# Performance work log

Hardware: AMD Instinct MI355X
Metric: run time of the kernel (lower is better)

## Reference

```python
import jax, jax.numpy as jnp
import numpy as np

N, F_IN, H, C, E = 100000, 128, 64, 40, 1600000
NEG_SLOPE = 0.2


def setup_inputs() -> dict:
    key = jax.random.key(0)
    ks = jax.random.split(key, 12)
    s = 0.1
    return {
        "x": jax.random.normal(ks[0], (N, F_IN), jnp.float32),
        "edge_index": jax.random.randint(ks[1], (2, E), 0, N, jnp.int32),
        "W1": jax.random.normal(ks[2], (F_IN, H), jnp.float32) * s,
        "a_src1": jax.random.normal(ks[3], (H,), jnp.float32) * s,
        "a_dst1": jax.random.normal(ks[4], (H,), jnp.float32) * s,
        "b1": jnp.zeros((H,), jnp.float32),
        "W2": jax.random.normal(ks[5], (H, H), jnp.float32) * s,
        "a_src2": jax.random.normal(ks[6], (H,), jnp.float32) * s,
        "a_dst2": jax.random.normal(ks[7], (H,), jnp.float32) * s,
        "b2": jnp.zeros((H,), jnp.float32),
        "Wl": jax.random.normal(ks[8], (H, C), jnp.float32) * s,
        "bl": jnp.zeros((C,), jnp.float32),
    }


def gat_conv(x, src, dst, W, a_src, a_dst, b):
    # PyG GATConv, heads=1, self-loops already appended to (src, dst)
    h = x @ W                                   # [N, H]
    alpha_s = h @ a_src                         # [N]
    alpha_d = h @ a_dst                         # [N]
    e = jax.nn.leaky_relu(alpha_s[src] + alpha_d[dst], NEG_SLOPE)  # [E]
    # segment softmax over incoming edges of each target node
    m = jax.ops.segment_max(e, dst, num_segments=x.shape[0])
    ex = jnp.exp(e - m[dst])
    denom = jax.ops.segment_sum(ex, dst, num_segments=x.shape[0])
    w = ex / (denom[dst] + 1e-16)               # [E]
    out = jax.ops.segment_sum(h[src] * w[:, None], dst, num_segments=x.shape[0])
    return out + b


def reference(x, edge_index, W1, a_src1, a_dst1, b1, W2, a_src2, a_dst2, b2, Wl, bl):
    n = x.shape[0]
    loops = jnp.arange(n, dtype=edge_index.dtype)
    src = jnp.concatenate([edge_index[0], loops])
    dst = jnp.concatenate([edge_index[1], loops])
    h = gat_conv(x, src, dst, W1, a_src1, a_dst1, b1)
    h = jax.nn.relu(h)  # dropout p=0 -> identity
    h = gat_conv(h, src, dst, W2, a_src2, a_dst2, b2)
    logits = h @ Wl + bl
    return jax.nn.log_softmax(logits, axis=-1)
```

## Files before the change

kernel.cpp:

```cpp
#include <hip/hip_runtime.h>
#include <math.h>


#define NEG_SLOPE 0.2f
#define NEG_BIG -3.0e38f

#define BSHIFT 9
#define BSIZE 512
#define BCAP 12288
#define EPB 4096

typedef __bf16 bf16x8 __attribute__((ext_vector_type(8)));
typedef __bf16 bf16x4 __attribute__((ext_vector_type(4)));
typedef float f32x4 __attribute__((ext_vector_type(4)));

__device__ __forceinline__ float lrelu(float x) {
    return x >= 0.f ? x : NEG_SLOPE * x;
}

__device__ __forceinline__ int wave_incl_scan(int v, int lane) {
#pragma unroll
    for (int d = 1; d < 64; d <<= 1) {
        int t = __shfl_up(v, d, 64);
        if (lane >= d) v += t;
    }
    return v;
}


__global__ __launch_bounds__(256) void fused_scatter_gemm(
        const int* __restrict__ src, const int* __restrict__ dst,
        int* __restrict__ bucketCount, unsigned* __restrict__ ebuf, int E, int SB,
        const float* __restrict__ X, const float* __restrict__ W,
        const float* __restrict__ a_src, const float* __restrict__ a_dst,
        __bf16* __restrict__ Hout, float* __restrict__ as_, float* __restrict__ ad_,
        int N, int nTiles) {
    constexpr int K = 128;
    __shared__ __bf16 Whi[64][K + 8];
    __shared__ __bf16 Wlo[64][K + 8];
    __shared__ int hist[256], base[256], cur[256];

    if (blockIdx.x < (unsigned)SB) {
        const int t = threadIdx.x;
        hist[t] = 0;
        __syncthreads();
        const int e0 = blockIdx.x * EPB;
        const int e1 = min(e0 + EPB, E);
        for (int e = e0 + t; e < e1; e += 256)
            atomicAdd(&hist[dst[e] >> BSHIFT], 1);
        __syncthreads();
        if (hist[t] > 0) base[t] = atomicAdd(&bucketCount[t], hist[t]);
        cur[t] = 0;
        __syncthreads();
        for (int e = e0 + t; e < e1; e += 256) {
            int d = dst[e];
            int b = d >> BSHIFT;
            int r = atomicAdd(&cur[b], 1);
            ebuf[(size_t)b * BCAP + base[b] + r] =
                ((unsigned)src[e] << BSHIFT) | (unsigned)(d & (BSIZE - 1));
        }
        return;
    }

    const int gbid = blockIdx.x - SB;
    for (int idx = threadIdx.x; idx < K * 64; idx += 256) {
        int k = idx >> 6, n = idx & 63;
        float w = W[idx];
        __bf16 hi = (__bf16)w;
        Whi[n][k] = hi;
        Wlo[n][k] = (__bf16)(w - (float)hi);
    }
    __syncthreads();

    const int lane  = threadIdx.x & 63;
    const int wave  = threadIdx.x >> 6;
    const int row16 = lane & 15;
    const int quad  = lane >> 4;

    float asv[4], adv[4];
#pragma unroll
    for (int t = 0; t < 4; ++t) {
        asv[t] = a_src[t * 16 + row16];
        adv[t] = a_dst[t * 16 + row16];
    }

    for (int tile = gbid; tile < nTiles; tile += 1024) {
        const int nbase = tile * 64;
        int gn = nbase + wave * 16 + row16;
        if (gn >= N) gn = N - 1;
        const float* __restrict__ xp = X + (size_t)gn * K + quad * 8;

        float4 xv[K / 16];
#pragma unroll
        for (int c = 0; c < K / 32; ++c) {
            xv[2 * c]     = *(const float4*)(xp + c * 32);
            xv[2 * c + 1] = *(const float4*)(xp + c * 32 + 4);
        }

        f32x4 acc[4] = {{0.f, 0.f, 0.f, 0.f}, {0.f, 0.f, 0.f, 0.f},
                        {0.f, 0.f, 0.f, 0.f}, {0.f, 0.f, 0.f, 0.f}};
#pragma unroll
        for (int kc = 0; kc < K; kc += 32) {
            float xs[8];
            *(float4*)&xs[0] = xv[kc / 16];
            *(float4*)&xs[4] = xv[kc / 16 + 1];
            bf16x8 ahi, alo;
#pragma unroll
            for (int j = 0; j < 8; ++j) {
                __bf16 hi = (__bf16)xs[j];
                ahi[j] = hi;
                alo[j] = (__bf16)(xs[j] - (float)hi);
            }
#pragma unroll
            for (int t = 0; t < 4; ++t) {
                bf16x8 bhi = *(const bf16x8*)&Whi[t * 16 + row16][kc + quad * 8];
                bf16x8 blo = *(const bf16x8*)&Wlo[t * 16 + row16][kc + quad * 8];
                acc[t] = __builtin_amdgcn_mfma_f32_16x16x32_bf16(ahi, bhi, acc[t], 0, 0, 0);
                acc[t] = __builtin_amdgcn_mfma_f32_16x16x32_bf16(ahi, blo, acc[t], 0, 0, 0);
                acc[t] = __builtin_amdgcn_mfma_f32_16x16x32_bf16(alo, bhi, acc[t], 0, 0, 0);
            }
        }

        float ps[4] = {0.f, 0.f, 0.f, 0.f};
        float pd[4] = {0.f, 0.f, 0.f, 0.f};
#pragma unroll
        for (int t = 0; t < 4; ++t) {
#pragma unroll
            for (int r = 0; r < 4; ++r) {
                int gm = nbase + wave * 16 + quad * 4 + r;
                if (gm < N) Hout[(size_t)gm * 64 + t * 16 + row16] = (__bf16)acc[t][r];
                ps[r] = fmaf(acc[t][r], asv[t], ps[r]);
                pd[r] = fmaf(acc[t][r], adv[t], pd[r]);
            }
        }
#pragma unroll
        for (int r = 0; r < 4; ++r) {
#pragma unroll
            for (int d = 1; d < 16; d <<= 1) {
                ps[r] += __shfl_xor(ps[r], d, 64);
                pd[r] += __shfl_xor(pd[r], d, 64);
            }
        }
        if (row16 == 0) {
#pragma unroll
            for (int r = 0; r < 4; ++r) {
                int gm = nbase + wave * 16 + quad * 4 + r;
                if (gm < N) { as_[gm] = ps[r]; ad_[gm] = pd[r]; }
            }
        }
    }
}


__global__ __launch_bounds__(512) void bucket_csr(const unsigned* __restrict__ ebuf,
                                                  const int* __restrict__ bucketCount,
                                                  int* __restrict__ offs,
                                                  int* __restrict__ csr, int N, int E) {
    __shared__ int hist[512], cursor[512], wsum[8];
    const int b = blockIdx.x;
    const int t = threadIdx.x;
    const int lane = t & 63;
    const int w = t >> 6;

    int v = (t < 256 && t < b) ? bucketCount[t] : 0;
#pragma unroll
    for (int d = 32; d; d >>= 1) v += __shfl_xor(v, d, 64);
    if (lane == 0) wsum[w] = v;
    hist[t] = 0;
    __syncthreads();
    int gbase = 0;
#pragma unroll
    for (int i = 0; i < 8; ++i) gbase += wsum[i];
    const int cnt = bucketCount[b];
    if (b == 0 && t == 0) offs[N] = E;

    const unsigned* __restrict__ eb = ebuf + (size_t)b * BCAP;
    for (int i = t; i < cnt; i += 512)
        atomicAdd(&hist[eb[i] & (BSIZE - 1)], 1);
    __syncthreads();

    int hv = hist[t];
    int incl = wave_incl_scan(hv, lane);
    if (lane == 63) wsum[w] = incl;
    __syncthreads();
    int prefix = 0;
    for (int i = 0; i < 8; ++i) prefix += (i < w) ? wsum[i] : 0;
    int excl = incl - hv + prefix;
    int n = b * BSIZE + t;
    if (n < N) offs[n] = gbase + excl;
    cursor[t] = excl;
    __syncthreads();

    for (int i = t; i < cnt; i += 512) {
        unsigned rec = eb[i];
        int pos = atomicAdd(&cursor[rec & (BSIZE - 1)], 1);
        csr[gbase + pos] = (int)(rec >> BSHIFT);
    }
}


__global__ __launch_bounds__(256) void gemm_mfma2(const __bf16* __restrict__ X,
                                                  const float* __restrict__ W,
                                                  const float* __restrict__ a_src,
                                                  const float* __restrict__ a_dst,
                                                  __bf16* __restrict__ Hout,
                                                  float* __restrict__ as_,
                                                  float* __restrict__ ad_,
                                                  int N, int nTiles) {
    constexpr int K = 64;
    __shared__ __bf16 Whi[64][K + 8];
    __shared__ __bf16 Wlo[64][K + 8];
    for (int idx = threadIdx.x; idx < K * 64; idx += 256) {
        int k = idx >> 6, n = idx & 63;
        float w = W[idx];
        __bf16 hi = (__bf16)w;
        Whi[n][k] = hi;
        Wlo[n][k] = (__bf16)(w - (float)hi);
    }
    __syncthreads();

    const int lane  = threadIdx.x & 63;
    const int wave  = threadIdx.x >> 6;
    const int row16 = lane & 15;
    const int quad  = lane >> 4;

    float asv[4], adv[4];
#pragma unroll
    for (int t = 0; t < 4; ++t) {
        asv[t] = a_src[t * 16 + row16];
        adv[t] = a_dst[t * 16 + row16];
    }

    for (int tile = blockIdx.x; tile < nTiles; tile += gridDim.x) {
        const int nbase = tile * 64;
        int gn = nbase + wave * 16 + row16;
        if (gn >= N) gn = N - 1;
        const __bf16* __restrict__ xp = X + (size_t)gn * K + quad * 8;
        bf16x8 a0 = *(const bf16x8*)(xp);
        bf16x8 a1 = *(const bf16x8*)(xp + 32);

        f32x4 acc[4] = {{0.f, 0.f, 0.f, 0.f}, {0.f, 0.f, 0.f, 0.f},
                        {0.f, 0.f, 0.f, 0.f}, {0.f, 0.f, 0.f, 0.f}};
#pragma unroll
        for (int kc = 0; kc < K; kc += 32) {
            bf16x8 a = (kc == 0) ? a0 : a1;
#pragma unroll
            for (int t = 0; t < 4; ++t) {
                bf16x8 bhi = *(const bf16x8*)&Whi[t * 16 + row16][kc + quad * 8];
                bf16x8 blo = *(const bf16x8*)&Wlo[t * 16 + row16][kc + quad * 8];
                acc[t] = __builtin_amdgcn_mfma_f32_16x16x32_bf16(a, bhi, acc[t], 0, 0, 0);
                acc[t] = __builtin_amdgcn_mfma_f32_16x16x32_bf16(a, blo, acc[t], 0, 0, 0);
            }
        }

        float ps[4] = {0.f, 0.f, 0.f, 0.f};
        float pd[4] = {0.f, 0.f, 0.f, 0.f};
#pragma unroll
        for (int t = 0; t < 4; ++t) {
#pragma unroll
            for (int r = 0; r < 4; ++r) {
                int gm = nbase + wave * 16 + quad * 4 + r;
                if (gm < N) Hout[(size_t)gm * 64 + t * 16 + row16] = (__bf16)acc[t][r];
                ps[r] = fmaf(acc[t][r], asv[t], ps[r]);
                pd[r] = fmaf(acc[t][r], adv[t], pd[r]);
            }
        }
#pragma unroll
        for (int r = 0; r < 4; ++r) {
#pragma unroll
            for (int d = 1; d < 16; d <<= 1) {
                ps[r] += __shfl_xor(ps[r], d, 64);
                pd[r] += __shfl_xor(pd[r], d, 64);
            }
        }
        if (row16 == 0) {
#pragma unroll
            for (int r = 0; r < 4; ++r) {
                int gm = nbase + wave * 16 + quad * 4 + r;
                if (gm < N) { as_[gm] = ps[r]; ad_[gm] = pd[r]; }
            }
        }
    }
}


__global__ __launch_bounds__(256) void gat_agg(const __bf16* __restrict__ h,
                                               const float* __restrict__ as_,
                                               const float* __restrict__ ad_,
                                               const float* __restrict__ bias,
                                               const int* __restrict__ offs,
                                               const int* __restrict__ csr,
                                               __bf16* __restrict__ out,
                                               int N, int do_relu) {
    int gtid = blockIdx.x * blockDim.x + threadIdx.x;
    int n = __builtin_amdgcn_readfirstlane(gtid >> 6);
    if (n >= N) return;
    const int lane = threadIdx.x & 63;
    const int g  = lane >> 3;
    const int fl = lane & 7;

    int beg = offs[n], end = offs[n + 1];
    float adn = ad_[n];
    float p_self = __expf(lrelu(as_[n] + adn));

    float den = p_self;
    float acc[8];
    {
        bf16x8 t = *(const bf16x8*)(h + (size_t)n * 64 + fl * 8);
        float m0 = (g == 0) ? p_self : 0.f;
#pragma unroll
        for (int i = 0; i < 8; ++i) acc[i] = m0 * (float)t[i];
    }

    for (int c0 = beg; c0 < end; c0 += 64) {
        int cnt = end - c0;
        if (cnt > 64) cnt = 64;
        int   s_l = (lane < cnt) ? csr[c0 + lane] : 0;
        float p_l = (lane < cnt) ? __expf(lrelu(as_[s_l] + adn)) : 0.f;
        float csum = p_l;
#pragma unroll
        for (int d = 32; d; d >>= 1) csum += __shfl_xor(csum, d, 64);
        den += csum;

        int rounds = (cnt + 7) >> 3;
        for (int r = 0; r < rounds; r += 4) {
            int j0 = (r + 0) * 8 + g, j1 = (r + 1) * 8 + g;
            int j2 = (r + 2) * 8 + g, j3 = (r + 3) * 8 + g;
            float w0 = __shfl(p_l, j0, 64), w1 = __shfl(p_l, j1, 64);
            float w2 = __shfl(p_l, j2, 64), w3 = __shfl(p_l, j3, 64);
            int s0 = __shfl(s_l, j0, 64), s1 = __shfl(s_l, j1, 64);
            int s2 = __shfl(s_l, j2, 64), s3 = __shfl(s_l, j3, 64);
            bf16x8 h0 = *(const bf16x8*)(h + (size_t)s0 * 64 + fl * 8);
            bf16x8 h1 = *(const bf16x8*)(h + (size_t)s1 * 64 + fl * 8);
            bf16x8 h2 = *(const bf16x8*)(h + (size_t)s2 * 64 + fl * 8);
            bf16x8 h3 = *(const bf16x8*)(h + (size_t)s3 * 64 + fl * 8);
#pragma unroll
            for (int i = 0; i < 8; ++i) {
                acc[i] = fmaf(w0, (float)h0[i], acc[i]);
                acc[i] = fmaf(w1, (float)h1[i], acc[i]);
                acc[i] = fmaf(w2, (float)h2[i], acc[i]);
                acc[i] = fmaf(w3, (float)h3[i], acc[i]);
            }
        }
    }

#pragma unroll
    for (int d = 8; d < 64; d <<= 1) {
#pragma unroll
        for (int i = 0; i < 8; ++i) acc[i] += __shfl_xor(acc[i], d, 64);
    }
    if (g == 0) {
        float inv = 1.f / (den + 1e-16f);
        float bv[8];
        *(float4*)&bv[0] = *(const float4*)(bias + fl * 8);
        *(float4*)&bv[4] = *(const float4*)(bias + fl * 8 + 4);
        bf16x8 ov;
#pragma unroll
        for (int i = 0; i < 8; ++i) {
            float o = fmaf(acc[i], inv, bv[i]);
            if (do_relu) o = fmaxf(o, 0.f);
            ov[i] = (__bf16)o;
        }
        *(bf16x8*)(out + (size_t)n * 64 + fl * 8) = ov;
    }
}


__global__ __launch_bounds__(256) void final_lsm(const __bf16* __restrict__ h,
                                                 const float* __restrict__ Wl,
                                                 const float* __restrict__ bl,
                                                 float* __restrict__ out,
                                                 int N, int nTiles) {
    __shared__ __bf16 Whi[48][72];
    __shared__ __bf16 Wlo[48][72];
    __shared__ float bls[48];
    for (int idx = threadIdx.x; idx < 48 * 64; idx += 256) {
        int c = idx >> 6, k = idx & 63;
        float w = (c < 40) ? Wl[k * 40 + c] : 0.f;
        __bf16 hi = (__bf16)w;
        Whi[c][k] = hi;
        Wlo[c][k] = (__bf16)(w - (float)hi);
    }
    if (threadIdx.x < 48) bls[threadIdx.x] = (threadIdx.x < 40) ? bl[threadIdx.x] : 0.f;
    __syncthreads();

    const int lane  = threadIdx.x & 63;
    const int wave  = threadIdx.x >> 6;
    const int col16 = lane & 15;
    const int quad  = lane >> 4;

    for (int tile = blockIdx.x; tile < nTiles; tile += gridDim.x) {
        const int nbase = tile * 64;
        int gn = nbase + wave * 16 + col16;
        if (gn >= N) gn = N - 1;
        const __bf16* __restrict__ xp = h + (size_t)gn * 64 + quad * 8;
        bf16x8 a0 = *(const bf16x8*)(xp);
        bf16x8 a1 = *(const bf16x8*)(xp + 32);

        f32x4 acc[3] = {{0.f, 0.f, 0.f, 0.f}, {0.f, 0.f, 0.f, 0.f},
                        {0.f, 0.f, 0.f, 0.f}};
#pragma unroll
        for (int kc = 0; kc < 64; kc += 32) {
            bf16x8 a = (kc == 0) ? a0 : a1;
#pragma unroll
            for (int t = 0; t < 3; ++t) {
                bf16x8 bhi = *(const bf16x8*)&Whi[t * 16 + col16][kc + quad * 8];
                bf16x8 blo = *(const bf16x8*)&Wlo[t * 16 + col16][kc + quad * 8];
                acc[t] = __builtin_amdgcn_mfma_f32_16x16x32_bf16(a, bhi, acc[t], 0, 0, 0);
                acc[t] = __builtin_amdgcn_mfma_f32_16x16x32_bf16(a, blo, acc[t], 0, 0, 0);
            }
        }

#pragma unroll
        for (int r = 0; r < 4; ++r) {
            int gm = nbase + wave * 16 + quad * 4 + r;
            float l0 = acc[0][r] + bls[col16];
            float l1 = acc[1][r] + bls[16 + col16];
            float l2 = (col16 < 8) ? (acc[2][r] + bls[32 + col16]) : NEG_BIG;
            float mx = fmaxf(fmaxf(l0, l1), l2);
#pragma unroll
            for (int d = 1; d < 16; d <<= 1) mx = fmaxf(mx, __shfl_xor(mx, d, 64));
            float s = __expf(l0 - mx) + __expf(l1 - mx) +
                      ((col16 < 8) ? __expf(l2 - mx) : 0.f);
#pragma unroll
            for (int d = 1; d < 16; d <<= 1) s += __shfl_xor(s, d, 64);
            float lse = mx + __logf(s);
            if (gm < N) {
                out[(size_t)gm * 40 + col16]      = l0 - lse;
                out[(size_t)gm * 40 + 16 + col16] = l1 - lse;
                if (col16 < 8) out[(size_t)gm * 40 + 32 + col16] = l2 - lse;
            }
        }
    }
}


extern "C" void kernel_launch(void* const* d_in, const int* in_sizes, int n_in,
                              void* d_out, int out_size, void* d_ws, size_t ws_size,
                              hipStream_t stream) {
    const float* x      = (const float*)d_in[0];
    const int*   ei     = (const int*)d_in[1];
    const float* W1     = (const float*)d_in[2];
    const float* a_src1 = (const float*)d_in[3];
    const float* a_dst1 = (const float*)d_in[4];
    const float* b1     = (const float*)d_in[5];
    const float* W2     = (const float*)d_in[6];
    const float* a_src2 = (const float*)d_in[7];
    const float* a_dst2 = (const float*)d_in[8];
    const float* b2     = (const float*)d_in[9];
    const float* Wl     = (const float*)d_in[10];
    const float* bl     = (const float*)d_in[11];

    const int N = in_sizes[0] / 128;
    const int E = in_sizes[1] / 2;
    const int* src = ei;
    const int* dst = ei + E;
    const int nbuck = (N + BSIZE - 1) >> BSHIFT;
    const int SB = (E + EPB - 1) / EPB;

    char* p = (char*)d_ws;
    auto alloc = [&](size_t bytes) -> void* {
        void* r = (void*)p;
        p += (bytes + 255) & ~(size_t)255;
        return r;
    };
    int*      offs        = (int*)alloc((size_t)(N + 1) * 4);
    int*      bucketCount = (int*)alloc(256 * 4);
    unsigned* ebuf        = (unsigned*)alloc((size_t)nbuck * BCAP * 4);
    int*      csr         = (int*)alloc((size_t)E * 4);
    __bf16*   hbf         = (__bf16*)alloc((size_t)N * 64 * 2);
    __bf16*   habg        = (__bf16*)alloc((size_t)N * 64 * 2);
    float*    as_         = (float*)alloc((size_t)N * 4);
    float*    ad_         = (float*)alloc((size_t)N * 4);

    hipMemsetAsync(bucketCount, 0, 256 * 4, stream);

    const int nTiles = (N + 63) / 64;
    int aggBlocks = (N * 64 + 255) / 256;

    fused_scatter_gemm<<<SB + 1024, 256, 0, stream>>>(
        src, dst, bucketCount, ebuf, E, SB,
        x, W1, a_src1, a_dst1, hbf, as_, ad_, N, nTiles);
    bucket_csr<<<nbuck, 512, 0, stream>>>(ebuf, bucketCount, offs, csr, N, E);
    gat_agg<<<aggBlocks, 256, 0, stream>>>(hbf, as_, ad_, b1, offs, csr, habg, N, 1);
    gemm_mfma2<<<1024, 256, 0, stream>>>(habg, W2, a_src2, a_dst2, hbf, as_, ad_, N, nTiles);
    gat_agg<<<aggBlocks, 256, 0, stream>>>(hbf, as_, ad_, b2, offs, csr, habg, N, 0);
    final_lsm<<<nTiles, 256, 0, stream>>>(habg, Wl, bl, (float*)d_out, N, nTiles);
}
```

Before: 300.7 us.

## Reuse histogram atomic ranks for scatter and switch aggregation to 4-edge groups

The bucket scatter and CSR build now keep the rank returned by the first histogram atomicAdd in registers and reuse it when placing each record, which removes the second pass of LDS atomics on a cursor array. The bucket scatter also writes with nontemporal stores. The GAT aggregation changes its lane mapping from 8 edges by 8 lanes of 8 features to 4 edges by 16 lanes of 4 features. This halves the per-edge accumulators and the cross-group shuffle reduction, at the cost of narrower 8-byte gathers and more loop rounds per chunk. The in-bucket ordering of records still depends on atomic order, as it did before.

```diff
diff --git a/kernel.cpp b/kernel.cpp
--- a/kernel.cpp
+++ b/kernel.cpp
@@ -38,7 +38,7 @@
     constexpr int K = 128;
     __shared__ __bf16 Whi[64][K + 8];
     __shared__ __bf16 Wlo[64][K + 8];
-    __shared__ int hist[256], base[256], cur[256];
+    __shared__ int hist[256], base[256];
 
     if (blockIdx.x < (unsigned)SB) {
         const int t = threadIdx.x;
@@ -46,18 +46,25 @@
         __syncthreads();
         const int e0 = blockIdx.x * EPB;
         const int e1 = min(e0 + EPB, E);
-        for (int e = e0 + t; e < e1; e += 256)
-            atomicAdd(&hist[dst[e] >> BSHIFT], 1);
+        int rr[EPB / 256];
+#pragma unroll
+        for (int i = 0; i < EPB / 256; ++i) {
+            int e = e0 + i * 256 + t;
+            if (e < e1) rr[i] = atomicAdd(&hist[dst[e] >> BSHIFT], 1);
+        }
         __syncthreads();
         if (hist[t] > 0) base[t] = atomicAdd(&bucketCount[t], hist[t]);
-        cur[t] = 0;
         __syncthreads();
-        for (int e = e0 + t; e < e1; e += 256) {
-            int d = dst[e];
-            int b = d >> BSHIFT;
-            int r = atomicAdd(&cur[b], 1);
-            ebuf[(size_t)b * BCAP + base[b] + r] =
-                ((unsigned)src[e] << BSHIFT) | (unsigned)(d & (BSIZE - 1));
+#pragma unroll
+        for (int i = 0; i < EPB / 256; ++i) {
+            int e = e0 + i * 256 + t;
+            if (e < e1) {
+                int d = dst[e];
+                int b = d >> BSHIFT;
+                __builtin_nontemporal_store(
+                    ((unsigned)src[e] << BSHIFT) | (unsigned)(d & (BSIZE - 1)),
+                    &ebuf[(size_t)b * BCAP + base[b] + rr[i]]);
+            }
         }
         return;
     }
@@ -156,7 +163,7 @@
                                                   const int* __restrict__ bucketCount,
                                                   int* __restrict__ offs,
                                                   int* __restrict__ csr, int N, int E) {
-    __shared__ int hist[512], cursor[512], wsum[8];
+    __shared__ int hist[512], excls[512], wsum[8];
     const int b = blockIdx.x;
     const int t = threadIdx.x;
     const int lane = t & 63;
@@ -175,8 +182,12 @@
     if (b == 0 && t == 0) offs[N] = E;
 
     const unsigned* __restrict__ eb = ebuf + (size_t)b * BCAP;
-    for (int i = t; i < cnt; i += 512)
-        atomicAdd(&hist[eb[i] & (BSIZE - 1)], 1);
+    int rr[BCAP / 512];
+#pragma unroll
+    for (int i = 0; i < BCAP / 512; ++i) {
+        int idx = i * 512 + t;
+        if (idx < cnt) rr[i] = atomicAdd(&hist[eb[idx] & (BSIZE - 1)], 1);
+    }
     __syncthreads();
 
     int hv = hist[t];
@@ -188,13 +199,16 @@
     int excl = incl - hv + prefix;
     int n = b * BSIZE + t;
     if (n < N) offs[n] = gbase + excl;
-    cursor[t] = excl;
-    __syncthreads();
-
-    for (int i = t; i < cnt; i += 512) {
-        unsigned rec = eb[i];
-        int pos = atomicAdd(&cursor[rec & (BSIZE - 1)], 1);
-        csr[gbase + pos] = (int)(rec >> BSHIFT);
+    excls[t] = excl;
+    __syncthreads();
+
+#pragma unroll
+    for (int i = 0; i < BCAP / 512; ++i) {
+        int idx = i * 512 + t;
+        if (idx < cnt) {
+            unsigned rec = eb[idx];
+            csr[gbase + excls[rec & (BSIZE - 1)] + rr[i]] = (int)(rec >> BSHIFT);
+        }
     }
 }
 
@@ -296,20 +310,22 @@
     int n = __builtin_amdgcn_readfirstlane(gtid >> 6);
     if (n >= N) return;
     const int lane = threadIdx.x & 63;
-    const int g  = lane >> 3;
-    const int fl = lane & 7;
+    const int g  = lane >> 4;
+    const int fl = lane & 15;
 
     int beg = offs[n], end = offs[n + 1];
     float adn = ad_[n];
     float p_self = __expf(lrelu(as_[n] + adn));
 
     float den = p_self;
-    float acc[8];
+    float ax, ay, az, aw;
     {
-        bf16x8 t = *(const bf16x8*)(h + (size_t)n * 64 + fl * 8);
+        bf16x4 t = *(const bf16x4*)(h + (size_t)n * 64 + fl * 4);
         float m0 = (g == 0) ? p_self : 0.f;
-#pragma unroll
-        for (int i = 0; i < 8; ++i) acc[i] = m0 * (float)t[i];
+        ax = m0 * (float)t[0];
+        ay = m0 * (float)t[1];
+        az = m0 * (float)t[2];
+        aw = m0 * (float)t[3];
     }
 
     for (int c0 = beg; c0 < end; c0 += 64) {
@@ -322,46 +338,51 @@
         for (int d = 32; d; d >>= 1) csum += __shfl_xor(csum, d, 64);
         den += csum;
 
-        int rounds = (cnt + 7) >> 3;
+        int rounds = (cnt + 3) >> 2;
         for (int r = 0; r < rounds; r += 4) {
-            int j0 = (r + 0) * 8 + g, j1 = (r + 1) * 8 + g;
-            int j2 = (r + 2) * 8 + g, j3 = (r + 3) * 8 + g;
+            int j0 = (r + 0) * 4 + g, j1 = (r + 1) * 4 + g;
+            int j2 = (r + 2) * 4 + g, j3 = (r + 3) * 4 + g;
             float w0 = __shfl(p_l, j0, 64), w1 = __shfl(p_l, j1, 64);
             float w2 = __shfl(p_l, j2, 64), w3 = __shfl(p_l, j3, 64);
             int s0 = __shfl(s_l, j0, 64), s1 = __shfl(s_l, j1, 64);
             int s2 = __shfl(s_l, j2, 64), s3 = __shfl(s_l, j3, 64);
-            bf16x8 h0 = *(const bf16x8*)(h + (size_t)s0 * 64 + fl * 8);
-            bf16x8 h1 = *(const bf16x8*)(h + (size_t)s1 * 64 + fl * 8);
-            bf16x8 h2 = *(const bf16x8*)(h + (size_t)s2 * 64 + fl * 8);
-            bf16x8 h3 = *(const bf16x8*)(h + (size_t)s3 * 64 + fl * 8);
-#pragma unroll
-            for (int i = 0; i < 8; ++i) {
-                acc[i] = fmaf(w0, (float)h0[i], acc[i]);
-                acc[i] = fmaf(w1, (float)h1[i], acc[i]);
-                acc[i] = fmaf(w2, (float)h2[i], acc[i]);
-                acc[i] = fmaf(w3, (float)h3[i], acc[i]);
-            }
-        }
-    }
-
-#pragma unroll
-    for (int d = 8; d < 64; d <<= 1) {
-#pragma unroll
-        for (int i = 0; i < 8; ++i) acc[i] += __shfl_xor(acc[i], d, 64);
+            bf16x4 h0 = *(const bf16x4*)(h + (size_t)s0 * 64 + fl * 4);
+            bf16x4 h1 = *(const bf16x4*)(h + (size_t)s1 * 64 + fl * 4);
+            bf16x4 h2 = *(const bf16x4*)(h + (size_t)s2 * 64 + fl * 4);
+            bf16x4 h3 = *(const bf16x4*)(h + (size_t)s3 * 64 + fl * 4);
+            ax = fmaf(w0, (float)h0[0], ax); ay = fmaf(w0, (float)h0[1], ay);
+            az = fmaf(w0, (float)h0[2], az); aw = fmaf(w0, (float)h0[3], aw);
+            ax = fmaf(w1, (float)h1[0], ax); ay = fmaf(w1, (float)h1[1], ay);
+            az = fmaf(w1, (float)h1[2], az); aw = fmaf(w1, (float)h1[3], aw);
+            ax = fmaf(w2, (float)h2[0], ax); ay = fmaf(w2, (float)h2[1], ay);
+            az = fmaf(w2, (float)h2[2], az); aw = fmaf(w2, (float)h2[3], aw);
+            ax = fmaf(w3, (float)h3[0], ax); ay = fmaf(w3, (float)h3[1], ay);
+            az = fmaf(w3, (float)h3[2], az); aw = fmaf(w3, (float)h3[3], aw);
+        }
+    }
+
+#pragma unroll
+    for (int d = 16; d <= 32; d <<= 1) {
+        ax += __shfl_xor(ax, d, 64);
+        ay += __shfl_xor(ay, d, 64);
+        az += __shfl_xor(az, d, 64);
+        aw += __shfl_xor(aw, d, 64);
     }
     if (g == 0) {
         float inv = 1.f / (den + 1e-16f);
-        float bv[8];
-        *(float4*)&bv[0] = *(const float4*)(bias + fl * 8);
-        *(float4*)&bv[4] = *(const float4*)(bias + fl * 8 + 4);
-        bf16x8 ov;
-#pragma unroll
-        for (int i = 0; i < 8; ++i) {
-            float o = fmaf(acc[i], inv, bv[i]);
-            if (do_relu) o = fmaxf(o, 0.f);
-            ov[i] = (__bf16)o;
-        }
-        *(bf16x8*)(out + (size_t)n * 64 + fl * 8) = ov;
+        const float4 b4 = *(const float4*)(bias + fl * 4);
+        bf16x4 ov;
+        float o0 = fmaf(ax, inv, b4.x);
+        float o1 = fmaf(ay, inv, b4.y);
+        float o2 = fmaf(az, inv, b4.z);
+        float o3 = fmaf(aw, inv, b4.w);
+        if (do_relu) {
+            o0 = fmaxf(o0, 0.f); o1 = fmaxf(o1, 0.f);
+            o2 = fmaxf(o2, 0.f); o3 = fmaxf(o3, 0.f);
+        }
+        ov[0] = (__bf16)o0; ov[1] = (__bf16)o1;
+        ov[2] = (__bf16)o2; ov[3] = (__bf16)o3;
+        *(bf16x4*)(out + (size_t)n * 64 + fl * 4) = ov;
     }
 }
 
```

New measurement: 317.1 us. +5.5%, slower.
